# Kernel tuning notes

Measured on AMD Instinct MI355X. Metric: run time of the kernel, lower is better.

The kernel has to match this reference:

```python
import jax, jax.numpy as jnp
import numpy as np

N_NODES = 50000
HEADS = 8
NEG_SLOPE = 0.2


def _gat_conv(x, src, dst, n, W, a_src, a_dst, b, concat):
    # W: [H*C, F_in], a_src/a_dst: [H, C], b: [H*C] or [C]
    H, C = a_src.shape
    h = (x @ W.T).reshape(-1, H, C)                      # [N, H, C]
    al_src = jnp.einsum('nhc,hc->nh', h, a_src)          # [N, H]
    al_dst = jnp.einsum('nhc,hc->nh', h, a_dst)          # [N, H]
    e = jax.nn.leaky_relu(al_src[src] + al_dst[dst], NEG_SLOPE)  # [E, H]
    # segment softmax over incoming edges of each dst node
    m = jax.lax.stop_gradient(jax.ops.segment_max(e, dst, num_segments=n))
    ee = jnp.exp(e - m[dst])
    denom = jax.ops.segment_sum(ee, dst, num_segments=n)
    alpha = ee / denom[dst]                              # [E, H]
    out = jax.ops.segment_sum(alpha[:, :, None] * h[src], dst, num_segments=n)  # [N, H, C]
    out = out.reshape(n, H * C) if concat else out.mean(axis=1)
    return out + b


def setup_inputs() -> dict:
    key = jax.random.key(0)
    ks = jax.random.split(key, 12)
    N, F_in, Hd, H, Ncls = N_NODES, 128, 32, HEADS, 40
    E = 800000
    x = jax.random.normal(ks[0], (N, F_in), dtype=jnp.float32)
    edge_index = jax.random.randint(ks[1], (2, E), 0, N, dtype=jnp.int64)
    s1 = 1.0 / np.sqrt(F_in)
    W1 = jax.random.normal(ks[2], (H * Hd, F_in), dtype=jnp.float32) * s1
    a_src1 = jax.random.normal(ks[3], (H, Hd), dtype=jnp.float32) * 0.1
    a_dst1 = jax.random.normal(ks[4], (H, Hd), dtype=jnp.float32) * 0.1
    b1 = jnp.zeros((H * Hd,), dtype=jnp.float32)
    s2 = 1.0 / np.sqrt(H * Hd)
    W2 = jax.random.normal(ks[5], (H * Ncls, H * Hd), dtype=jnp.float32) * s2
    a_src2 = jax.random.normal(ks[6], (H, Ncls), dtype=jnp.float32) * 0.1
    a_dst2 = jax.random.normal(ks[7], (H, Ncls), dtype=jnp.float32) * 0.1
    b2 = jnp.zeros((Ncls,), dtype=jnp.float32)
    return {"x": x, "edge_index": edge_index,
            "W1": W1, "a_src1": a_src1, "a_dst1": a_dst1, "b1": b1,
            "W2": W2, "a_src2": a_src2, "a_dst2": a_dst2, "b2": b2}


def reference(x, edge_index, W1, a_src1, a_dst1, b1, W2, a_src2, a_dst2, b2):
    n = x.shape[0]
    # PyG GATConv default: add self loops
    loop = jnp.arange(n, dtype=edge_index.dtype)
    src = jnp.concatenate([edge_index[0], loop])
    dst = jnp.concatenate([edge_index[1], loop])
    # layer 1 (concat heads) -> ELU; dropout identity in eval mode
    h = _gat_conv(x, src, dst, n, W1, a_src1, a_dst1, b1, concat=True)
    h = jax.nn.elu(h)
    # layer 2 (mean over heads)
    out = _gat_conv(h, src, dst, n, W2, a_src2, a_dst2, b2, concat=False)
    return jax.nn.log_softmax(out, axis=1)
```

## Files before the change

kernel.cpp:

```cpp
#include <hip/hip_runtime.h>
#include <hip/hip_bf16.h>
#include <math.h>

typedef unsigned short ushort_t;
typedef unsigned char uchar_t;
typedef __attribute__((ext_vector_type(8))) short short8;
typedef __attribute__((ext_vector_type(4))) float f32x4;
typedef __attribute__((ext_vector_type(2))) float f32x2;
typedef __attribute__((ext_vector_type(4))) unsigned short u16x4;

static __device__ __forceinline__ float b2f(ushort_t u) {
    union { unsigned int i; float f; } v; v.i = ((unsigned int)u) << 16; return v.f;
}
static __device__ __forceinline__ ushort_t f2b(float f) {
    unsigned int x = __float_as_uint(f);
    unsigned int r = (x + 0x7fffu + ((x >> 16) & 1u)) >> 16;
    return (ushort_t)r;
}
static __device__ __forceinline__ uchar_t f2e4m3(float f) {
    int r = __builtin_amdgcn_cvt_pk_fp8_f32(f, f, 0, false);
    return (uchar_t)(r & 0xff);
}


__global__ void conv_kernel(const float* __restrict__ src, ushort_t* __restrict__ dst, int n4) {
    for (int i = blockIdx.x * blockDim.x + threadIdx.x; i < n4; i += gridDim.x * blockDim.x) {
        float4 v = *(const float4*)(src + i * 4);
        u16x4 o = { f2b(v.x), f2b(v.y), f2b(v.z), f2b(v.w) };
        *(u16x4*)(dst + i * 4) = o;
    }
}

template<int K, int Cd>
__global__ void build_wa(const float* __restrict__ W, const float* __restrict__ as,
                         const float* __restrict__ ad, ushort_t* __restrict__ Bext, int rowoff) {
    int tid = blockIdx.x * blockDim.x + threadIdx.x;
    if (tid >= 16 * K) return;
    int col = tid / K, k = tid - col * K;
    const float* a = (col < 8) ? as : ad;
    int h = col & 7;
    float s = 0.f;
    #pragma unroll 4
    for (int c = 0; c < Cd; ++c)
        s += W[(size_t)(h * Cd + c) * K + k] * a[h * Cd + c];
    Bext[(size_t)(rowoff + col) * K + k] = f2b(s);
}

__global__ void pad_row_kernel(float* als1, float* als2, uchar_t* h1f8, uchar_t* h2f8, int n) {
    int t = threadIdx.x;
    if (t < 8) { als1[(size_t)n * 8 + t] = -1e30f; als2[(size_t)n * 8 + t] = -1e30f; }
    if (t < 256) h1f8[(size_t)n * 256 + t] = 0;
    if (t < 320) h2f8[(size_t)n * 320 + t] = 0;
}


__global__ void count_kernel(const int* __restrict__ ei, int E, int n, int* __restrict__ deg) {
    int e = blockIdx.x * blockDim.x + threadIdx.x;
    int Etot = E + n;
    if (e >= Etot) return;
    int dst = (e < E) ? ei[E + e] : (e - E);
    atomicAdd(&deg[dst], 1);
}

__global__ void scan_kernel(const int* __restrict__ deg, int* __restrict__ rowptr,
                            int* __restrict__ cursor, int n) {
    __shared__ int wsum[16];
    int t = threadIdx.x;
    int lane = t & 63, wid = t >> 6;
    int carry = 0;
    for (int base = 0; base < n; base += 1024) {
        int i = base + t;
        int v = (i < n) ? ((deg[i] + 7) & ~7) : 0;
        int val = v;
        #pragma unroll
        for (int off = 1; off < 64; off <<= 1) {
            int nv = __shfl_up(val, off);
            if (lane >= off) val += nv;
        }
        if (lane == 63) wsum[wid] = val;
        __syncthreads();
        int wpre = 0, tot = 0;
        #pragma unroll
        for (int w = 0; w < 16; ++w) {
            int s = wsum[w];
            if (w < wid) wpre += s;
            tot += s;
        }
        int excl = carry + wpre + val - v;
        if (i < n) { rowptr[i] = excl; cursor[i] = excl; }
        carry += tot;
        __syncthreads();
    }
    if (t == 0) rowptr[n] = carry;
}

__global__ void scatter_kernel(const int* __restrict__ ei, int E, int n,
                               int* __restrict__ cursor, int* __restrict__ ssrc) {
    int e = blockIdx.x * blockDim.x + threadIdx.x;
    int Etot = E + n;
    if (e >= Etot) return;
    int src, dst;
    if (e < E) { src = ei[e]; dst = ei[E + e]; }
    else       { src = e - E; dst = e - E; }
    int pos = atomicAdd(&cursor[dst], 1);
    ssrc[pos] = src;
}

__global__ void pad_fill_kernel(const int* __restrict__ rowptr, const int* __restrict__ cursor,
                                int* __restrict__ ssrc, int n) {
    int i = blockIdx.x * blockDim.x + threadIdx.x;
    if (i >= n) return;
    int p = cursor[i], e = rowptr[i + 1];
    for (; p < e; ++p) ssrc[p] = n;
}


template<int NFRAG, int K>
__global__ __launch_bounds__(512) void gemm_lds_al(const ushort_t* __restrict__ A,
                                                   const ushort_t* __restrict__ B,
                                                   uchar_t* __restrict__ C,
                                                   float* __restrict__ als,
                                                   float* __restrict__ ald, int M) {
    constexpr int N = NFRAG * 16;
    constexpr int NOUT = (NFRAG - 1) * 16;
    constexpr int RS = 40;
    constexpr int NK = K / 32;
    __shared__ ushort_t Bs[2][N * RS];
    const int t = threadIdx.x;
    const int w = t >> 6, l = t & 63;
    const int r0 = blockIdx.x * 128 + w * 16;
    int arow = r0 + (l & 15);
    if (arow >= M) arow = M - 1;
    const int koff = (l >> 4) * 8;
    const ushort_t* ap = A + (size_t)arow * K + koff;

    f32x4 acc[NFRAG];
    #pragma unroll
    for (int i = 0; i < NFRAG; ++i) acc[i] = (f32x4){0.f, 0.f, 0.f, 0.f};

    auto stage = [&](int buf, int k0) {
        #pragma unroll
        for (int c = t; c < N * 4; c += 512) {
            int row = c >> 2, part = (c & 3) << 3;
            *(short8*)&Bs[buf][row * RS + part] =
                *(const short8*)(B + (size_t)row * K + k0 + part);
        }
    };

    stage(0, 0);
    __syncthreads();
    #pragma unroll
    for (int kk = 0; kk < NK; ++kk) {
        int buf = kk & 1;
        if (kk + 1 < NK) stage(buf ^ 1, (kk + 1) * 32);
        short8 a = *(const short8*)(ap + kk * 32);
        #pragma unroll
        for (int nf = 0; nf < NFRAG; ++nf) {
            short8 b = *(const short8*)&Bs[buf][(nf * 16 + (l & 15)) * RS + koff];
            acc[nf] = __builtin_amdgcn_mfma_f32_16x16x32_bf16(a, b, acc[nf], 0, 0, 0);
        }
        __syncthreads();
    }

    const int crow0 = r0 + (l >> 4) * 4;
    #pragma unroll
    for (int nf = 0; nf < NFRAG - 1; ++nf) {
        #pragma unroll
        for (int j = 0; j < 4; ++j) {
            int row = crow0 + j;
            if (row < M) C[(size_t)row * NOUT + nf * 16 + (l & 15)] = f2e4m3(acc[nf][j]);
        }
    }
    {
        int col = l & 15;
        float* dstp = (col < 8) ? als : ald;
        int h = col & 7;
        #pragma unroll
        for (int j = 0; j < 4; ++j) {
            int row = crow0 + j;
            if (row < M) dstp[(size_t)row * 8 + h] = acc[NFRAG - 1][j];
        }
    }
}


__device__ __forceinline__ float lrelu(float e) { return (e > 0.f) ? e : 0.2f * e; }

__global__ void agg1_kernel(const uchar_t* __restrict__ h1, const float* __restrict__ als,
                            const float* __restrict__ aldv, const float* __restrict__ b1,
                            const int* __restrict__ rowptr, const int* __restrict__ ssrc,
                            ushort_t* __restrict__ hout, int n) {
    int node = blockIdx.x * 4 + (threadIdx.x >> 6);
    if (node >= n) return;
    int l = threadIdx.x & 63;
    int h = l >> 3;
    float ald = aldv[node * 8 + h];
    int beg = rowptr[node], end = rowptr[node + 1];
    float m = -1e30f, den = 0.f, a0 = 0.f, a1 = 0.f, a2 = 0.f, a3 = 0.f;
    for (int p = beg; p < end; p += 8) {
        int4 sA = *(const int4*)(ssrc + p);
        int4 sB = *(const int4*)(ssrc + p + 4);
        float e0 = lrelu(als[sA.x * 8 + h] + ald);
        float e1 = lrelu(als[sA.y * 8 + h] + ald);
        float e2 = lrelu(als[sA.z * 8 + h] + ald);
        float e3 = lrelu(als[sA.w * 8 + h] + ald);
        float e4 = lrelu(als[sB.x * 8 + h] + ald);
        float e5 = lrelu(als[sB.y * 8 + h] + ald);
        float e6 = lrelu(als[sB.z * 8 + h] + ald);
        float e7 = lrelu(als[sB.w * 8 + h] + ald);
        int g0 = *(const int*)(h1 + (size_t)sA.x * 256 + l * 4);
        int g1 = *(const int*)(h1 + (size_t)sA.y * 256 + l * 4);
        int g2 = *(const int*)(h1 + (size_t)sA.z * 256 + l * 4);
        int g3 = *(const int*)(h1 + (size_t)sA.w * 256 + l * 4);
        int g4 = *(const int*)(h1 + (size_t)sB.x * 256 + l * 4);
        int g5 = *(const int*)(h1 + (size_t)sB.y * 256 + l * 4);
        int g6 = *(const int*)(h1 + (size_t)sB.z * 256 + l * 4);
        int g7 = *(const int*)(h1 + (size_t)sB.w * 256 + l * 4);
        float em = fmaxf(fmaxf(fmaxf(e0, e1), fmaxf(e2, e3)),
                         fmaxf(fmaxf(e4, e5), fmaxf(e6, e7)));
        if (em > m + 8.f) {
            float f = __expf(m - em);
            den *= f; a0 *= f; a1 *= f; a2 *= f; a3 *= f;
            m = em;
        }
        float w0 = __expf(e0 - m), w1 = __expf(e1 - m);
        float w2 = __expf(e2 - m), w3 = __expf(e3 - m);
        float w4 = __expf(e4 - m), w5 = __expf(e5 - m);
        float w6 = __expf(e6 - m), w7 = __expf(e7 - m);
        den += ((w0 + w1) + (w2 + w3)) + ((w4 + w5) + (w6 + w7));
        #define DQ(g, wv) { \
            f32x2 lo = __builtin_amdgcn_cvt_pk_f32_fp8(g, false); \
            f32x2 hi = __builtin_amdgcn_cvt_pk_f32_fp8(g, true);  \
            a0 += wv * lo.x; a1 += wv * lo.y; a2 += wv * hi.x; a3 += wv * hi.y; }
        DQ(g0, w0) DQ(g1, w1) DQ(g2, w2) DQ(g3, w3)
        DQ(g4, w4) DQ(g5, w5) DQ(g6, w6) DQ(g7, w7)
        #undef DQ
    }
    float inv = 1.f / den;
    float4 bv = *(const float4*)(b1 + l * 4);
    float v0 = a0 * inv + bv.x, v1 = a1 * inv + bv.y;
    float v2 = a2 * inv + bv.z, v3 = a3 * inv + bv.w;
    u16x4 o;
    o.x = f2b((v0 > 0.f) ? v0 : __expf(v0) - 1.f);
    o.y = f2b((v1 > 0.f) ? v1 : __expf(v1) - 1.f);
    o.z = f2b((v2 > 0.f) ? v2 : __expf(v2) - 1.f);
    o.w = f2b((v3 > 0.f) ? v3 : __expf(v3) - 1.f);
    *(u16x4*)(hout + (size_t)node * 256 + l * 4) = o;
}


__global__ void agg2_kernel(const uchar_t* __restrict__ h2, const float* __restrict__ als,
                            const float* __restrict__ aldv, const float* __restrict__ b2,
                            const int* __restrict__ rowptr, const int* __restrict__ ssrc,
                            float* __restrict__ out, int n) {
    int node = blockIdx.x * 4 + (threadIdx.x >> 6);
    if (node >= n) return;
    int l = threadIdx.x & 63;
    int li = (l < 40) ? l : 0;
    int hd = li / 5;
    int cg = li - hd * 5;
    float ald = aldv[node * 8 + hd];
    int beg = rowptr[node], end = rowptr[node + 1];
    const uchar_t* base = h2 + hd * 40 + cg * 8;
    float m = -1e30f, den = 0.f;
    float a0 = 0.f, a1 = 0.f, a2 = 0.f, a3 = 0.f, a4 = 0.f, a5 = 0.f, a6 = 0.f, a7 = 0.f;
    for (int p = beg; p < end; p += 8) {
        int4 sA = *(const int4*)(ssrc + p);
        int4 sB = *(const int4*)(ssrc + p + 4);
        float e0 = lrelu(als[sA.x * 8 + hd] + ald);
        float e1 = lrelu(als[sA.y * 8 + hd] + ald);
        float e2 = lrelu(als[sA.z * 8 + hd] + ald);
        float e3 = lrelu(als[sA.w * 8 + hd] + ald);
        float e4 = lrelu(als[sB.x * 8 + hd] + ald);
        float e5 = lrelu(als[sB.y * 8 + hd] + ald);
        float e6 = lrelu(als[sB.z * 8 + hd] + ald);
        float e7 = lrelu(als[sB.w * 8 + hd] + ald);
        uint2 g0 = *(const uint2*)(base + (size_t)sA.x * 320);
        uint2 g1 = *(const uint2*)(base + (size_t)sA.y * 320);
        uint2 g2 = *(const uint2*)(base + (size_t)sA.z * 320);
        uint2 g3 = *(const uint2*)(base + (size_t)sA.w * 320);
        uint2 g4 = *(const uint2*)(base + (size_t)sB.x * 320);
        uint2 g5 = *(const uint2*)(base + (size_t)sB.y * 320);
        uint2 g6 = *(const uint2*)(base + (size_t)sB.z * 320);
        uint2 g7 = *(const uint2*)(base + (size_t)sB.w * 320);
        float em = fmaxf(fmaxf(fmaxf(e0, e1), fmaxf(e2, e3)),
                         fmaxf(fmaxf(e4, e5), fmaxf(e6, e7)));
        if (em > m + 8.f) {
            float f = __expf(m - em);
            den *= f;
            a0 *= f; a1 *= f; a2 *= f; a3 *= f; a4 *= f; a5 *= f; a6 *= f; a7 *= f;
            m = em;
        }
        float w0 = __expf(e0 - m), w1 = __expf(e1 - m);
        float w2 = __expf(e2 - m), w3 = __expf(e3 - m);
        float w4 = __expf(e4 - m), w5 = __expf(e5 - m);
        float w6 = __expf(e6 - m), w7 = __expf(e7 - m);
        den += ((w0 + w1) + (w2 + w3)) + ((w4 + w5) + (w6 + w7));
        #define DQ(g, wv) { \
            f32x2 q0 = __builtin_amdgcn_cvt_pk_f32_fp8((int)g.x, false); \
            f32x2 q1 = __builtin_amdgcn_cvt_pk_f32_fp8((int)g.x, true);  \
            f32x2 q2 = __builtin_amdgcn_cvt_pk_f32_fp8((int)g.y, false); \
            f32x2 q3 = __builtin_amdgcn_cvt_pk_f32_fp8((int)g.y, true);  \
            a0 += wv * q0.x; a1 += wv * q0.y; a2 += wv * q1.x; a3 += wv * q1.y; \
            a4 += wv * q2.x; a5 += wv * q2.y; a6 += wv * q3.x; a7 += wv * q3.y; }
        DQ(g0, w0) DQ(g1, w1) DQ(g2, w2) DQ(g3, w3)
        DQ(g4, w4) DQ(g5, w5) DQ(g6, w6) DQ(g7, w7)
        #undef DQ
    }
    float inv = 1.f / den;
    float v[8] = {a0 * inv, a1 * inv, a2 * inv, a3 * inv,
                  a4 * inv, a5 * inv, a6 * inv, a7 * inv};
    #pragma unroll
    for (int j = 0; j < 8; ++j) {
        float s = v[j];
        s += __shfl_down(s, 20);
        s += __shfl_down(s, 10);
        s += __shfl_down(s, 5);
        v[j] = s;
    }
    if (l < 5) {
        float wv[8];
        #pragma unroll
        for (int j = 0; j < 8; ++j) wv[j] = 0.125f * v[j] + b2[l * 8 + j];
        float m8 = wv[0];
        #pragma unroll
        for (int j = 1; j < 8; ++j) m8 = fmaxf(m8, wv[j]);
        float mx = m8;
        #pragma unroll
        for (int k = 0; k < 5; ++k) mx = fmaxf(mx, __shfl(m8, k));
        float se8 = 0.f;
        #pragma unroll
        for (int j = 0; j < 8; ++j) se8 += __expf(wv[j] - mx);
        float se = 0.f;
        #pragma unroll
        for (int k = 0; k < 5; ++k) se += __shfl(se8, k);
        float lse = mx + __logf(se);
        float* op = out + (size_t)node * 40 + l * 8;
        float4 o0 = {wv[0] - lse, wv[1] - lse, wv[2] - lse, wv[3] - lse};
        float4 o1 = {wv[4] - lse, wv[5] - lse, wv[6] - lse, wv[7] - lse};
        *(float4*)op = o0;
        *(float4*)(op + 4) = o1;
    }
}


extern "C" void kernel_launch(void* const* d_in, const int* in_sizes, int n_in,
                              void* d_out, int out_size, void* d_ws, size_t ws_size,
                              hipStream_t stream) {
    const float* x      = (const float*)d_in[0];
    const int*   ei     = (const int*)d_in[1];
    const float* W1     = (const float*)d_in[2];
    const float* a_src1 = (const float*)d_in[3];
    const float* a_dst1 = (const float*)d_in[4];
    const float* b1     = (const float*)d_in[5];
    const float* W2     = (const float*)d_in[6];
    const float* a_src2 = (const float*)d_in[7];
    const float* a_dst2 = (const float*)d_in[8];
    const float* b2     = (const float*)d_in[9];
    float* out = (float*)d_out;

    const int n    = in_sizes[0] / 128;
    const int E    = in_sizes[1] / 2;
    const int Etot = E + n;
    const int EpM  = Etot + 7 * n + 16;

    char* w = (char*)d_ws;
    auto take = [&](size_t bytes) {
        char* p = w;
        w += (bytes + 255) & ~(size_t)255;
        return p;
    };
    int*      deg    = (int*)take((size_t)n * 4);
    int*      rowptr = (int*)take((size_t)(n + 1) * 4);
    int*      cursor = (int*)take((size_t)n * 4);
    int*      ssrc   = (int*)take((size_t)EpM * 4);
    ushort_t* xb     = (ushort_t*)take((size_t)n * 128 * 2);
    ushort_t* w1b    = (ushort_t*)take((size_t)272 * 128 * 2);
    ushort_t* w2b    = (ushort_t*)take((size_t)336 * 256 * 2);
    uchar_t*  h1f8   = (uchar_t*)take((size_t)(n + 1) * 256);
    ushort_t* helu   = (ushort_t*)take((size_t)n * 256 * 2);
    uchar_t*  h2f8   = (uchar_t*)take((size_t)(n + 1) * 320);
    float*    als1   = (float*)take((size_t)(n + 1) * 8 * 4);
    float*    ald1   = (float*)take((size_t)n * 8 * 4);
    float*    als2   = (float*)take((size_t)(n + 1) * 8 * 4);
    float*    ald2   = (float*)take((size_t)n * 8 * 4);

    hipMemsetAsync(deg, 0, (size_t)n * 4, stream);
    pad_row_kernel<<<1, 512, 0, stream>>>(als1, als2, h1f8, h2f8, n);

    conv_kernel<<<2048, 256, 0, stream>>>(x, xb, n * 128 / 4);
    conv_kernel<<<32, 256, 0, stream>>>(W1, w1b, 256 * 128 / 4);
    conv_kernel<<<80, 256, 0, stream>>>(W2, w2b, 320 * 256 / 4);
    build_wa<128, 32><<<8, 256, 0, stream>>>(W1, a_src1, a_dst1, w1b, 256);
    build_wa<256, 40><<<16, 256, 0, stream>>>(W2, a_src2, a_dst2, w2b, 320);

    int eb = (Etot + 255) / 256;
    count_kernel<<<eb, 256, 0, stream>>>(ei, E, n, deg);
    scan_kernel<<<1, 1024, 0, stream>>>(deg, rowptr, cursor, n);
    scatter_kernel<<<eb, 256, 0, stream>>>(ei, E, n, cursor, ssrc);
    pad_fill_kernel<<<(n + 255) / 256, 256, 0, stream>>>(rowptr, cursor, ssrc, n);

    int gb = (n + 127) / 128;
    int nb4 = (n + 3) / 4;

    gemm_lds_al<17, 128><<<gb, 512, 0, stream>>>(xb, w1b, h1f8, als1, ald1, n);
    agg1_kernel<<<nb4, 256, 0, stream>>>(h1f8, als1, ald1, b1, rowptr, ssrc, helu, n);

    gemm_lds_al<21, 256><<<gb, 512, 0, stream>>>(helu, w2b, h2f8, als2, ald2, n);
    agg2_kernel<<<nb4, 256, 0, stream>>>(h2f8, als2, ald2, b2, rowptr, ssrc, out, n);
}
```

Baseline: 308.0 us.

## Drop online-max softmax via log2-prescaled logits; compute two row tiles per GEMM wave

```diff
diff --git a/kernel.cpp b/kernel.cpp
--- a/kernel.cpp
+++ b/kernel.cpp
@@ -9,6 +9,8 @@
 typedef __attribute__((ext_vector_type(2))) float f32x2;
 typedef __attribute__((ext_vector_type(4))) unsigned short u16x4;
 
+#define LOG2E 1.44269504088896f
+
 static __device__ __forceinline__ float b2f(ushort_t u) {
     union { unsigned int i; float f; } v; v.i = ((unsigned int)u) << 16; return v.f;
 }
@@ -20,6 +22,9 @@
 static __device__ __forceinline__ uchar_t f2e4m3(float f) {
     int r = __builtin_amdgcn_cvt_pk_fp8_f32(f, f, 0, false);
     return (uchar_t)(r & 0xff);
+}
+static __device__ __forceinline__ float exp2fast(float x) {
+    return __builtin_amdgcn_exp2f(x);
 }
 
 
@@ -43,7 +48,7 @@
     #pragma unroll 4
     for (int c = 0; c < Cd; ++c)
         s += W[(size_t)(h * Cd + c) * K + k] * a[h * Cd + c];
-    Bext[(size_t)(rowoff + col) * K + k] = f2b(s);
+    Bext[(size_t)(rowoff + col) * K + k] = f2b(s * LOG2E);
 }
 
 __global__ void pad_row_kernel(float* als1, float* als2, uchar_t* h1f8, uchar_t* h2f8, int n) {
@@ -128,15 +133,21 @@
     __shared__ ushort_t Bs[2][N * RS];
     const int t = threadIdx.x;
     const int w = t >> 6, l = t & 63;
-    const int r0 = blockIdx.x * 128 + w * 16;
-    int arow = r0 + (l & 15);
-    if (arow >= M) arow = M - 1;
+    const int r0 = blockIdx.x * 256 + w * 32;
+    int arow0 = r0 + (l & 15);
+    int arow1 = r0 + 16 + (l & 15);
+    if (arow0 >= M) arow0 = M - 1;
+    if (arow1 >= M) arow1 = M - 1;
     const int koff = (l >> 4) * 8;
-    const ushort_t* ap = A + (size_t)arow * K + koff;
-
-    f32x4 acc[NFRAG];
+    const ushort_t* ap0 = A + (size_t)arow0 * K + koff;
+    const ushort_t* ap1 = A + (size_t)arow1 * K + koff;
+
+    f32x4 acc0[NFRAG], acc1[NFRAG];
     #pragma unroll
-    for (int i = 0; i < NFRAG; ++i) acc[i] = (f32x4){0.f, 0.f, 0.f, 0.f};
+    for (int i = 0; i < NFRAG; ++i) {
+        acc0[i] = (f32x4){0.f, 0.f, 0.f, 0.f};
+        acc1[i] = (f32x4){0.f, 0.f, 0.f, 0.f};
+    }
 
     auto stage = [&](int buf, int k0) {
         #pragma unroll
@@ -153,11 +164,13 @@
     for (int kk = 0; kk < NK; ++kk) {
         int buf = kk & 1;
         if (kk + 1 < NK) stage(buf ^ 1, (kk + 1) * 32);
-        short8 a = *(const short8*)(ap + kk * 32);
+        short8 a0 = *(const short8*)(ap0 + kk * 32);
+        short8 a1 = *(const short8*)(ap1 + kk * 32);
         #pragma unroll
         for (int nf = 0; nf < NFRAG; ++nf) {
             short8 b = *(const short8*)&Bs[buf][(nf * 16 + (l & 15)) * RS + koff];
-            acc[nf] = __builtin_amdgcn_mfma_f32_16x16x32_bf16(a, b, acc[nf], 0, 0, 0);
+            acc0[nf] = __builtin_amdgcn_mfma_f32_16x16x32_bf16(a0, b, acc0[nf], 0, 0, 0);
+            acc1[nf] = __builtin_amdgcn_mfma_f32_16x16x32_bf16(a1, b, acc1[nf], 0, 0, 0);
         }
         __syncthreads();
     }
@@ -167,8 +180,9 @@
     for (int nf = 0; nf < NFRAG - 1; ++nf) {
         #pragma unroll
         for (int j = 0; j < 4; ++j) {
-            int row = crow0 + j;
-            if (row < M) C[(size_t)row * NOUT + nf * 16 + (l & 15)] = f2e4m3(acc[nf][j]);
+            int row0 = crow0 + j, row1 = crow0 + 16 + j;
+            if (row0 < M) C[(size_t)row0 * NOUT + nf * 16 + (l & 15)] = f2e4m3(acc0[nf][j]);
+            if (row1 < M) C[(size_t)row1 * NOUT + nf * 16 + (l & 15)] = f2e4m3(acc1[nf][j]);
         }
     }
     {
@@ -177,8 +191,9 @@
         int h = col & 7;
         #pragma unroll
         for (int j = 0; j < 4; ++j) {
-            int row = crow0 + j;
-            if (row < M) dstp[(size_t)row * 8 + h] = acc[NFRAG - 1][j];
+            int row0 = crow0 + j, row1 = crow0 + 16 + j;
+            if (row0 < M) dstp[(size_t)row0 * 8 + h] = acc0[NFRAG - 1][j];
+            if (row1 < M) dstp[(size_t)row1 * 8 + h] = acc1[NFRAG - 1][j];
         }
     }
 }
@@ -196,18 +211,18 @@
     int h = l >> 3;
     float ald = aldv[node * 8 + h];
     int beg = rowptr[node], end = rowptr[node + 1];
-    float m = -1e30f, den = 0.f, a0 = 0.f, a1 = 0.f, a2 = 0.f, a3 = 0.f;
+    float den = 0.f, a0 = 0.f, a1 = 0.f, a2 = 0.f, a3 = 0.f;
     for (int p = beg; p < end; p += 8) {
         int4 sA = *(const int4*)(ssrc + p);
         int4 sB = *(const int4*)(ssrc + p + 4);
-        float e0 = lrelu(als[sA.x * 8 + h] + ald);
-        float e1 = lrelu(als[sA.y * 8 + h] + ald);
-        float e2 = lrelu(als[sA.z * 8 + h] + ald);
-        float e3 = lrelu(als[sA.w * 8 + h] + ald);
-        float e4 = lrelu(als[sB.x * 8 + h] + ald);
-        float e5 = lrelu(als[sB.y * 8 + h] + ald);
-        float e6 = lrelu(als[sB.z * 8 + h] + ald);
-        float e7 = lrelu(als[sB.w * 8 + h] + ald);
+        float w0 = exp2fast(lrelu(als[sA.x * 8 + h] + ald));
+        float w1 = exp2fast(lrelu(als[sA.y * 8 + h] + ald));
+        float w2 = exp2fast(lrelu(als[sA.z * 8 + h] + ald));
+        float w3 = exp2fast(lrelu(als[sA.w * 8 + h] + ald));
+        float w4 = exp2fast(lrelu(als[sB.x * 8 + h] + ald));
+        float w5 = exp2fast(lrelu(als[sB.y * 8 + h] + ald));
+        float w6 = exp2fast(lrelu(als[sB.z * 8 + h] + ald));
+        float w7 = exp2fast(lrelu(als[sB.w * 8 + h] + ald));
         int g0 = *(const int*)(h1 + (size_t)sA.x * 256 + l * 4);
         int g1 = *(const int*)(h1 + (size_t)sA.y * 256 + l * 4);
         int g2 = *(const int*)(h1 + (size_t)sA.z * 256 + l * 4);
@@ -216,17 +231,6 @@
         int g5 = *(const int*)(h1 + (size_t)sB.y * 256 + l * 4);
         int g6 = *(const int*)(h1 + (size_t)sB.z * 256 + l * 4);
         int g7 = *(const int*)(h1 + (size_t)sB.w * 256 + l * 4);
-        float em = fmaxf(fmaxf(fmaxf(e0, e1), fmaxf(e2, e3)),
-                         fmaxf(fmaxf(e4, e5), fmaxf(e6, e7)));
-        if (em > m + 8.f) {
-            float f = __expf(m - em);
-            den *= f; a0 *= f; a1 *= f; a2 *= f; a3 *= f;
-            m = em;
-        }
-        float w0 = __expf(e0 - m), w1 = __expf(e1 - m);
-        float w2 = __expf(e2 - m), w3 = __expf(e3 - m);
-        float w4 = __expf(e4 - m), w5 = __expf(e5 - m);
-        float w6 = __expf(e6 - m), w7 = __expf(e7 - m);
         den += ((w0 + w1) + (w2 + w3)) + ((w4 + w5) + (w6 + w7));
         #define DQ(g, wv) { \
             f32x2 lo = __builtin_amdgcn_cvt_pk_f32_fp8(g, false); \
@@ -262,19 +266,19 @@
     float ald = aldv[node * 8 + hd];
     int beg = rowptr[node], end = rowptr[node + 1];
     const uchar_t* base = h2 + hd * 40 + cg * 8;
-    float m = -1e30f, den = 0.f;
+    float den = 0.f;
     float a0 = 0.f, a1 = 0.f, a2 = 0.f, a3 = 0.f, a4 = 0.f, a5 = 0.f, a6 = 0.f, a7 = 0.f;
     for (int p = beg; p < end; p += 8) {
         int4 sA = *(const int4*)(ssrc + p);
         int4 sB = *(const int4*)(ssrc + p + 4);
-        float e0 = lrelu(als[sA.x * 8 + hd] + ald);
-        float e1 = lrelu(als[sA.y * 8 + hd] + ald);
-        float e2 = lrelu(als[sA.z * 8 + hd] + ald);
-        float e3 = lrelu(als[sA.w * 8 + hd] + ald);
-        float e4 = lrelu(als[sB.x * 8 + hd] + ald);
-        float e5 = lrelu(als[sB.y * 8 + hd] + ald);
-        float e6 = lrelu(als[sB.z * 8 + hd] + ald);
-        float e7 = lrelu(als[sB.w * 8 + hd] + ald);
+        float w0 = exp2fast(lrelu(als[sA.x * 8 + hd] + ald));
+        float w1 = exp2fast(lrelu(als[sA.y * 8 + hd] + ald));
+        float w2 = exp2fast(lrelu(als[sA.z * 8 + hd] + ald));
+        float w3 = exp2fast(lrelu(als[sA.w * 8 + hd] + ald));
+        float w4 = exp2fast(lrelu(als[sB.x * 8 + hd] + ald));
+        float w5 = exp2fast(lrelu(als[sB.y * 8 + hd] + ald));
+        float w6 = exp2fast(lrelu(als[sB.z * 8 + hd] + ald));
+        float w7 = exp2fast(lrelu(als[sB.w * 8 + hd] + ald));
         uint2 g0 = *(const uint2*)(base + (size_t)sA.x * 320);
         uint2 g1 = *(const uint2*)(base + (size_t)sA.y * 320);
         uint2 g2 = *(const uint2*)(base + (size_t)sA.z * 320);
@@ -283,18 +287,6 @@
         uint2 g5 = *(const uint2*)(base + (size_t)sB.y * 320);
         uint2 g6 = *(const uint2*)(base + (size_t)sB.z * 320);
         uint2 g7 = *(const uint2*)(base + (size_t)sB.w * 320);
-        float em = fmaxf(fmaxf(fmaxf(e0, e1), fmaxf(e2, e3)),
-                         fmaxf(fmaxf(e4, e5), fmaxf(e6, e7)));
-        if (em > m + 8.f) {
-            float f = __expf(m - em);
-            den *= f;
-            a0 *= f; a1 *= f; a2 *= f; a3 *= f; a4 *= f; a5 *= f; a6 *= f; a7 *= f;
-            m = em;
-        }
-        float w0 = __expf(e0 - m), w1 = __expf(e1 - m);
-        float w2 = __expf(e2 - m), w3 = __expf(e3 - m);
-        float w4 = __expf(e4 - m), w5 = __expf(e5 - m);
-        float w6 = __expf(e6 - m), w7 = __expf(e7 - m);
         den += ((w0 + w1) + (w2 + w3)) + ((w4 + w5) + (w6 + w7));
         #define DQ(g, wv) { \
             f32x2 q0 = __builtin_amdgcn_cvt_pk_f32_fp8((int)g.x, false); \
@@ -400,7 +392,7 @@
     scatter_kernel<<<eb, 256, 0, stream>>>(ei, E, n, cursor, ssrc);
     pad_fill_kernel<<<(n + 255) / 256, 256, 0, stream>>>(rowptr, cursor, ssrc, n);
 
-    int gb = (n + 127) / 128;
+    int gb = (n + 255) / 256;
     int nb4 = (n + 3) / 4;
 
     gemm_lds_al<17, 128><<<gb, 512, 0, stream>>>(xb, w1b, h1f8, als1, ald1, n);
```

Result: no change. 306.3 us (-0.5%).
